# Kernel optimization log

Measured on AMD Instinct MI355X. Metric: run time of the kernel, lower is better.

## Reference

```python
import jax, jax.numpy as jnp
import numpy as np

N = 100000
F = 256
H = 128
C = 64
E = 1600000

def spmm(rows, cols, vals, h):
    # sparse [N,N] @ dense [N,D] via gather + segment-sum
    return jax.ops.segment_sum(vals[:, None] * h[cols], rows, num_segments=N)

def graph_conv(x, W, rows, cols, vals, b=None):
    # GraphConv: support = x @ W; out = adj @ support (+ bias)
    out = spmm(rows, cols, vals, x @ W)
    if b is not None:
        out = out + b
    return out

def setup_inputs() -> dict:
    key = jax.random.key(0)
    ks = jax.random.split(key, 20)
    d = {}
    d['x'] = jax.random.normal(ks[0], (N, F), dtype=jnp.float32)
    for i, name in enumerate(['mid', 'low', 'high']):
        d[name + '_rows'] = jax.random.randint(ks[1 + 3 * i], (E,), 0, N, dtype=jnp.int64 if jax.config.jax_enable_x64 else jnp.int32)
        d[name + '_cols'] = jax.random.randint(ks[2 + 3 * i], (E,), 0, N, dtype=jnp.int64 if jax.config.jax_enable_x64 else jnp.int32)
        d[name + '_vals'] = jax.random.uniform(ks[3 + 3 * i], (E,), dtype=jnp.float32) * 0.1
    s = lambda k, a, b_: jax.random.normal(k, (a, b_), dtype=jnp.float32) * (1.0 / np.sqrt(a))
    d['W_hid'] = s(ks[10], F, H)          # hidden_layers[0], no bias
    d['W_out'] = s(ks[11], H, C)          # out_layer
    d['b_out'] = jnp.zeros((C,), jnp.float32)
    d['W_low'] = s(ks[12], F, H)          # addHid_layer, no bias
    d['W_low_out'] = s(ks[13], H, C)      # addOut_layer
    d['b_low_out'] = jnp.zeros((C,), jnp.float32)
    d['W_high'] = s(ks[14], F, H)         # addHid_layer_HIGH, no bias
    d['W_high_out'] = s(ks[15], H, C)     # addOut_layer_HIGH
    d['b_high_out'] = jnp.zeros((C,), jnp.float32)
    d['gate2'] = jnp.array([0.5], jnp.float32)
    return d

def reference(x, mid_rows, mid_cols, mid_vals, low_rows, low_cols, low_vals,
              high_rows, high_cols, high_vals, W_hid, W_out, b_out,
              W_low, W_low_out, b_low_out, W_high, W_high_out, b_high_out, gate2):
    # dropout is identity at inference
    h = jax.nn.relu(graph_conv(x, W_hid, mid_rows, mid_cols, mid_vals))
    h = graph_conv(h, W_out, mid_rows, mid_cols, mid_vals, b_out)
    x2 = jax.nn.relu(graph_conv(x, W_low, low_rows, low_cols, low_vals))
    xh = jax.nn.relu(graph_conv(x, W_high, high_rows, high_cols, high_vals))
    x2 = graph_conv(x2, W_low_out, low_rows, low_cols, low_vals, b_low_out)
    xh = graph_conv(xh, W_high_out, high_rows, high_cols, high_vals, b_high_out)
    x_final = gate2 * h + (1.0 - gate2) * (x2 + xh)
    return jax.nn.log_softmax(x_final, axis=-1)
```

## Files before the change

### kernel.cpp

```cpp
#include <hip/hip_runtime.h>
#include <math.h>

#define NNODES 100000
#define NEDGES 1600000
#define FEAT 256
#define HID 128
#define NCLS 64
#define RPB 512
#define NBG 196
#define NB3 (3 * NBG)
#define CAP 8832
#define SC_CHUNK 8192
#define SC_THREADS 1024

typedef __attribute__((ext_vector_type(8))) short bf16x8;
typedef __attribute__((ext_vector_type(4))) float f32x4;
typedef __attribute__((ext_vector_type(2))) float f32x2;

__device__ __forceinline__ float bf2f(unsigned int u16) {
  union { unsigned int i; float f; } c; c.i = u16 << 16; return c.f;
}
__device__ __forceinline__ unsigned short f2bf(float f) {
  union { float f; unsigned int i; } c; c.f = f;
  unsigned int u = c.i;
  return (unsigned short)((u + 0x7fffu + ((u >> 16) & 1u)) >> 16);
}

__device__ __forceinline__ void fma8(const uint4 u, const f32x2 vv, f32x2* a) {
  f32x2 p0, p1, p2, p3;
  p0.x = __uint_as_float(u.x << 16); p0.y = __uint_as_float(u.x & 0xffff0000u);
  p1.x = __uint_as_float(u.y << 16); p1.y = __uint_as_float(u.y & 0xffff0000u);
  p2.x = __uint_as_float(u.z << 16); p2.y = __uint_as_float(u.z & 0xffff0000u);
  p3.x = __uint_as_float(u.w << 16); p3.y = __uint_as_float(u.w & 0xffff0000u);
  a[0] += p0 * vv; a[1] += p1 * vv; a[2] += p2 * vv; a[3] += p3 * vv;
}

__global__ __launch_bounds__(SC_THREADS) void k_bucket_scatter(
    const int* __restrict__ r0, const int* __restrict__ r1, const int* __restrict__ r2,
    const int* __restrict__ c0, const int* __restrict__ c1, const int* __restrict__ c2,
    const float* __restrict__ v0, const float* __restrict__ v1, const float* __restrict__ v2,
    int* __restrict__ gcur, int2* __restrict__ edges) {
  __shared__ int2 stage[SC_CHUNK];
  __shared__ unsigned char bid[SC_CHUNK];
  __shared__ int hist[NBG];
  __shared__ int lbase[NBG];
  __shared__ int gstart[NBG];
  __shared__ int cur[NBG];
  __shared__ int sd[2][256];
  int g = blockIdx.y;
  const int*   rr = (g == 0) ? r0 : (g == 1 ? r1 : r2);
  const int*   cc = (g == 0) ? c0 : (g == 1 ? c1 : c2);
  const float* vv = (g == 0) ? v0 : (g == 1 ? v1 : v2);
  int tid = threadIdx.x;
  int base = blockIdx.x * SC_CHUNK;
  int cnt_blk = NEDGES - base;
  if (cnt_blk > SC_CHUNK) cnt_blk = SC_CHUNK;

  for (int i = tid; i < NBG; i += SC_THREADS) hist[i] = 0;
  __syncthreads();

  int rowv[SC_CHUNK / SC_THREADS];
  int colv[SC_CHUNK / SC_THREADS];
  float valv[SC_CHUNK / SC_THREADS];
#pragma unroll
  for (int k = 0; k < SC_CHUNK / SC_THREADS; k++) {
    int e = base + k * SC_THREADS + tid;
    bool ok = e < NEDGES;
    rowv[k] = ok ? rr[e] : -1;
    colv[k] = ok ? cc[e] : 0;
    valv[k] = ok ? vv[e] : 0.f;
    if (ok) atomicAdd(&hist[rowv[k] >> 9], 1);
  }
  __syncthreads();

  if (tid < 256) sd[0][tid] = (tid < NBG) ? hist[tid] : 0;
  __syncthreads();
  int c = 0;
  for (int off = 1; off < 256; off <<= 1) {
    if (tid < 256) {
      int nv = sd[c][tid];
      if (tid >= off) nv += sd[c][tid - off];
      sd[c ^ 1][tid] = nv;
    }
    __syncthreads();
    c ^= 1;
  }
  if (tid < NBG) {
    int cn = hist[tid];
    int excl = sd[c][tid] - cn;
    lbase[tid] = excl;
    cur[tid] = excl;
    gstart[tid] = cn ? atomicAdd(&gcur[g * NBG + tid], cn) : 0;
  }
  __syncthreads();

#pragma unroll
  for (int k = 0; k < SC_CHUNK / SC_THREADS; k++) {
    if (rowv[k] >= 0) {
      int b = rowv[k] >> 9;
      int p = atomicAdd(&cur[b], 1);
      stage[p] = make_int2(((rowv[k] & (RPB - 1)) << 17) | colv[k], __float_as_int(valv[k]));
      bid[p] = (unsigned char)b;
    }
  }
  __syncthreads();

  for (int i = tid; i < cnt_blk; i += SC_THREADS) {
    int b = bid[i];
    int pos = gstart[b] + (i - lbase[b]);
    if (pos < CAP)
      edges[(size_t)(g * NBG + b) * CAP + pos] = stage[i];
  }
}

__global__ __launch_bounds__(512) void k_bucket_sort(const int* __restrict__ gcur,
                                                     int2* __restrict__ edges,
                                                     int* __restrict__ rps_all,
                                                     int* __restrict__ rpe_all) {
  __shared__ int2 stage[CAP];
  __shared__ int hist[RPB];
  __shared__ int sd[2][RPB];
  __shared__ int cur[RPB];
  int g = blockIdx.y, b = blockIdx.x;
  int tid = threadIdx.x;
  int idx = g * NBG + b;
  size_t base = (size_t)idx * CAP;
  int count = gcur[idx];
  if (count > CAP) count = CAP;
  hist[tid] = 0;
  __syncthreads();

  const int KSL = (CAP + 511) / 512;
  int2 ev[KSL];
#pragma unroll
  for (int k = 0; k < KSL; k++) {
    int i = tid + k * 512;
    if (i < count) {
      ev[k] = edges[base + i];
      atomicAdd(&hist[ev[k].x >> 17], 1);
    }
  }
  __syncthreads();

  int v = hist[tid];
  sd[0][tid] = v;
  __syncthreads();
  int c2 = 0;
  for (int off = 1; off < 512; off <<= 1) {
    int nv = sd[c2][tid];
    if (tid >= off) nv += sd[c2][tid - off];
    sd[c2 ^ 1][tid] = nv;
    __syncthreads();
    c2 ^= 1;
  }
  int excl = sd[c2][tid] - v;
  int row = b * RPB + tid;
  if (row < NNODES) {
    rps_all[g * NNODES + row] = (int)base + excl;
    rpe_all[g * NNODES + row] = (int)base + excl + v;
  }
  cur[tid] = excl;
  __syncthreads();

#pragma unroll
  for (int k = 0; k < KSL; k++) {
    int i = tid + k * 512;
    if (i < count) {
      int lr = ev[k].x >> 17;
      int p = atomicAdd(&cur[lr], 1);
      stage[p] = make_int2(ev[k].x & 0x1FFFF, ev[k].y);
    }
  }
  __syncthreads();

  for (int i = tid; i < count; i += 512) edges[base + i] = stage[i];
}

__global__ __launch_bounds__(256) void k_convert_bf16(const float* __restrict__ src,
                                                      unsigned short* __restrict__ dst,
                                                      int n4) {
  int i = blockIdx.x * blockDim.x + threadIdx.x;
  if (i < n4) {
    float4 v = ((const float4*)src)[i];
    ushort4 o;
    o.x = f2bf(v.x); o.y = f2bf(v.y); o.z = f2bf(v.z); o.w = f2bf(v.w);
    ((ushort4*)dst)[i] = o;
  }
}

__global__ __launch_bounds__(256) void k_transpose3(const float* __restrict__ s0,
                                                    const float* __restrict__ s1,
                                                    const float* __restrict__ s2,
                                                    unsigned short* __restrict__ d0,
                                                    unsigned short* __restrict__ d1,
                                                    unsigned short* __restrict__ d2,
                                                    int K, int N) {
  int g = blockIdx.y;
  const float* src = (g == 0) ? s0 : (g == 1 ? s1 : s2);
  unsigned short* dst = (g == 0) ? d0 : (g == 1 ? d1 : d2);
  int idx = blockIdx.x * 256 + threadIdx.x;
  if (idx < K * N) {
    int k = idx / N, n = idx % N;
    dst[(size_t)n * K + k] = f2bf(src[idx]);
  }
}

__global__ __launch_bounds__(256) void k_gemm1_b(const unsigned short* __restrict__ A,
                                                 const unsigned short* __restrict__ WtA,
                                                 unsigned short* __restrict__ C3, int M) {
  int bxy = blockIdx.x;
  int g = bxy % 3;
  int bx = bxy / 3;
  const unsigned short* Wt = WtA + (size_t)g * HID * FEAT;
  unsigned short* C = C3 + (size_t)g * M * HID;
  int tid = threadIdx.x;
  int wave = tid >> 6, lane = tid & 63;
  int quad = lane >> 4, r = lane & 15;
  int m0 = bx * 128 + wave * 32;
  int ra0 = m0 + r;      if (ra0 >= M) ra0 = 0;
  int ra1 = m0 + 16 + r; if (ra1 >= M) ra1 = 0;
  const unsigned short* pa0 = A + (size_t)ra0 * FEAT + quad * 8;
  const unsigned short* pa1 = A + (size_t)ra1 * FEAT + quad * 8;
  f32x4 acc[2][8];
#pragma unroll
  for (int i = 0; i < 2; i++)
#pragma unroll
    for (int j = 0; j < 8; j++) acc[i][j] = (f32x4){0.f, 0.f, 0.f, 0.f};
  for (int k0 = 0; k0 < FEAT; k0 += 32) {
    bf16x8 a0 = *(const bf16x8*)(pa0 + k0);
    bf16x8 a1 = *(const bf16x8*)(pa1 + k0);
#pragma unroll
    for (int nt = 0; nt < 8; nt++) {
      bf16x8 b = *(const bf16x8*)(Wt + (size_t)(nt * 16 + r) * FEAT + k0 + quad * 8);
      acc[0][nt] = __builtin_amdgcn_mfma_f32_16x16x32_bf16(a0, b, acc[0][nt], 0, 0, 0);
      acc[1][nt] = __builtin_amdgcn_mfma_f32_16x16x32_bf16(a1, b, acc[1][nt], 0, 0, 0);
    }
  }
#pragma unroll
  for (int t = 0; t < 2; t++)
#pragma unroll
    for (int reg = 0; reg < 4; reg++) {
      int row = m0 + t * 16 + quad * 4 + reg;
      if (row < M) {
#pragma unroll
        for (int nt = 0; nt < 8; nt++)
          C[(size_t)row * HID + nt * 16 + r] = f2bf(acc[t][nt][reg]);
      }
    }
}

__global__ __launch_bounds__(256) void k_gemm2_b(const unsigned short* __restrict__ A3,
                                                 const unsigned short* __restrict__ WtA,
                                                 unsigned short* __restrict__ C3, int M) {
  int g = blockIdx.y;
  const unsigned short* A = A3 + (size_t)g * M * HID;
  const unsigned short* Wt = WtA + (size_t)g * NCLS * HID;
  unsigned short* C = C3 + (size_t)g * M * NCLS;
  int tid = threadIdx.x;
  int wave = tid >> 6, lane = tid & 63;
  int quad = lane >> 4, r = lane & 15;
  int m0 = blockIdx.x * 128 + wave * 32;
  int ra0 = m0 + r;      if (ra0 >= M) ra0 = 0;
  int ra1 = m0 + 16 + r; if (ra1 >= M) ra1 = 0;
  const unsigned short* pa0 = A + (size_t)ra0 * HID + quad * 8;
  const unsigned short* pa1 = A + (size_t)ra1 * HID + quad * 8;
  f32x4 acc[2][4];
#pragma unroll
  for (int i = 0; i < 2; i++)
#pragma unroll
    for (int j = 0; j < 4; j++) acc[i][j] = (f32x4){0.f, 0.f, 0.f, 0.f};
  for (int k0 = 0; k0 < HID; k0 += 32) {
    bf16x8 a0 = *(const bf16x8*)(pa0 + k0);
    bf16x8 a1 = *(const bf16x8*)(pa1 + k0);
#pragma unroll
    for (int nt = 0; nt < 4; nt++) {
      bf16x8 b = *(const bf16x8*)(Wt + (size_t)(nt * 16 + r) * HID + k0 + quad * 8);
      acc[0][nt] = __builtin_amdgcn_mfma_f32_16x16x32_bf16(a0, b, acc[0][nt], 0, 0, 0);
      acc[1][nt] = __builtin_amdgcn_mfma_f32_16x16x32_bf16(a1, b, acc[1][nt], 0, 0, 0);
    }
  }
#pragma unroll
  for (int t = 0; t < 2; t++)
#pragma unroll
    for (int reg = 0; reg < 4; reg++) {
      int row = m0 + t * 16 + quad * 4 + reg;
      if (row < M) {
#pragma unroll
        for (int nt = 0; nt < 4; nt++)
          C[(size_t)row * NCLS + nt * 16 + r] = f2bf(acc[t][nt][reg]);
      }
    }
}

__global__ __launch_bounds__(256) void k_spmm128_b(const int* __restrict__ rps_all,
                                                   const int* __restrict__ rpe_all,
                                                   const int2* __restrict__ edges,
                                                   const unsigned short* __restrict__ dense3,
                                                   unsigned short* __restrict__ out3, int n) {
  int g = blockIdx.y;
  const int* rs = rps_all + (size_t)g * NNODES;
  const int* re = rpe_all + (size_t)g * NNODES;
  const unsigned short* dense = dense3 + (size_t)g * NNODES * HID;
  unsigned short* out = out3 + (size_t)g * NNODES * HID;
  int w = (blockIdx.x * blockDim.x + threadIdx.x) >> 6;
  int lane = threadIdx.x & 63;
  if (w >= n) return;
  int grp = lane >> 4;
  int sub = lane & 15;
  int s = rs[w], e = re[w];
  f32x2 a[4][4];
#pragma unroll
  for (int t = 0; t < 4; t++)
#pragma unroll
    for (int q = 0; q < 4; q++) a[t][q] = (f32x2){0.f, 0.f};
  for (int j = s; j < e; j += 16) {
    uint4 u[4];
    float f[4];
#pragma unroll
    for (int t = 0; t < 4; t++) {
      int ej = j + t * 4 + grp;
      bool ok = ej < e;
      int2 dd = edges[ok ? ej : s];
      u[t] = *(const uint4*)(dense + (size_t)dd.x * HID + sub * 8);
      f[t] = ok ? __int_as_float(dd.y) : 0.f;
    }
#pragma unroll
    for (int t = 0; t < 4; t++) {
      f32x2 vv; vv.x = f[t]; vv.y = f[t];
      fma8(u[t], vv, a[t]);
    }
  }
  unsigned int pk[4];
#pragma unroll
  for (int q = 0; q < 4; q++) {
    float lo = (a[0][q].x + a[1][q].x) + (a[2][q].x + a[3][q].x);
    float hi = (a[0][q].y + a[1][q].y) + (a[2][q].y + a[3][q].y);
    lo += __shfl_xor(lo, 32, 64); lo += __shfl_xor(lo, 16, 64);
    hi += __shfl_xor(hi, 32, 64); hi += __shfl_xor(hi, 16, 64);
    lo = fmaxf(lo, 0.f); hi = fmaxf(hi, 0.f);
    pk[q] = (unsigned int)f2bf(lo) | ((unsigned int)f2bf(hi) << 16);
  }
  if (lane < 16) {
    uint4 o; o.x = pk[0]; o.y = pk[1]; o.z = pk[2]; o.w = pk[3];
    *(uint4*)(out + (size_t)w * HID + sub * 8) = o;
  }
}

__global__ __launch_bounds__(256) void k_spmm64_final(const int* __restrict__ rps_all,
                                                      const int* __restrict__ rpe_all,
                                                      const int2* __restrict__ edges,
                                                      const unsigned short* __restrict__ dense3,
                                                      const float* __restrict__ b0p,
                                                      const float* __restrict__ b1p,
                                                      const float* __restrict__ b2p,
                                                      const float* __restrict__ gate,
                                                      float* __restrict__ outp, int n) {
  int w = (blockIdx.x * blockDim.x + threadIdx.x) >> 6;
  int lane = threadIdx.x & 63;
  if (w >= n) return;
  int grp = lane >> 3;
  int sub = lane & 7;
  float gv = gate[0];
  float omg = 1.0f - gv;
  float tot[8];
  {
    float4 x0 = *(const float4*)(b0p + sub * 8), x1 = *(const float4*)(b0p + sub * 8 + 4);
    float4 y0 = *(const float4*)(b1p + sub * 8), y1 = *(const float4*)(b1p + sub * 8 + 4);
    float4 z0 = *(const float4*)(b2p + sub * 8), z1 = *(const float4*)(b2p + sub * 8 + 4);
    tot[0] = gv * x0.x + omg * (y0.x + z0.x); tot[1] = gv * x0.y + omg * (y0.y + z0.y);
    tot[2] = gv * x0.z + omg * (y0.z + z0.z); tot[3] = gv * x0.w + omg * (y0.w + z0.w);
    tot[4] = gv * x1.x + omg * (y1.x + z1.x); tot[5] = gv * x1.y + omg * (y1.y + z1.y);
    tot[6] = gv * x1.z + omg * (y1.z + z1.z); tot[7] = gv * x1.w + omg * (y1.w + z1.w);
  }
  for (int g = 0; g < 3; g++) {
    const int* rs = rps_all + (size_t)g * NNODES;
    const int* re = rpe_all + (size_t)g * NNODES;
    const unsigned short* dense = dense3 + (size_t)g * NNODES * NCLS;
    int s = rs[w], e = re[w];
    f32x2 a0[4], a1[4];
#pragma unroll
    for (int q = 0; q < 4; q++) { a0[q] = (f32x2){0.f, 0.f}; a1[q] = (f32x2){0.f, 0.f}; }
    for (int j = s; j < e; j += 16) {
      int e0 = j + grp, e1 = j + 8 + grp;
      bool k0 = e0 < e, k1 = e1 < e;
      int2 d0 = edges[k0 ? e0 : s];
      int2 d1 = edges[k1 ? e1 : s];
      uint4 u0 = *(const uint4*)(dense + (size_t)d0.x * NCLS + sub * 8);
      uint4 u1 = *(const uint4*)(dense + (size_t)d1.x * NCLS + sub * 8);
      float f0 = k0 ? __int_as_float(d0.y) : 0.f;
      float f1 = k1 ? __int_as_float(d1.y) : 0.f;
      f32x2 v0; v0.x = f0; v0.y = f0;
      f32x2 v1; v1.x = f1; v1.y = f1;
      fma8(u0, v0, a0);
      fma8(u1, v1, a1);
    }
    float scale = (g == 0) ? gv : omg;
#pragma unroll
    for (int q = 0; q < 4; q++) {
      float lo = a0[q].x + a1[q].x;
      float hi = a0[q].y + a1[q].y;
      lo += __shfl_xor(lo, 32, 64); lo += __shfl_xor(lo, 16, 64); lo += __shfl_xor(lo, 8, 64);
      hi += __shfl_xor(hi, 32, 64); hi += __shfl_xor(hi, 16, 64); hi += __shfl_xor(hi, 8, 64);
      tot[2 * q] += scale * lo;
      tot[2 * q + 1] += scale * hi;
    }
  }
  float m = tot[0];
#pragma unroll
  for (int i = 1; i < 8; i++) m = fmaxf(m, tot[i]);
  m = fmaxf(m, __shfl_xor(m, 1, 64));
  m = fmaxf(m, __shfl_xor(m, 2, 64));
  m = fmaxf(m, __shfl_xor(m, 4, 64));
  float sum = 0.f;
#pragma unroll
  for (int i = 0; i < 8; i++) sum += expf(tot[i] - m);
  sum += __shfl_xor(sum, 1, 64);
  sum += __shfl_xor(sum, 2, 64);
  sum += __shfl_xor(sum, 4, 64);
  float ls = m + logf(sum);
  if (grp == 0) {
    size_t o = (size_t)w * NCLS + sub * 8;
    *(float4*)(outp + o)     = make_float4(tot[0] - ls, tot[1] - ls, tot[2] - ls, tot[3] - ls);
    *(float4*)(outp + o + 4) = make_float4(tot[4] - ls, tot[5] - ls, tot[6] - ls, tot[7] - ls);
  }
}

extern "C" void kernel_launch(void* const* d_in, const int* in_sizes, int n_in,
                              void* d_out, int out_size, void* d_ws, size_t ws_size,
                              hipStream_t stream) {
  (void)in_sizes; (void)n_in; (void)out_size; (void)ws_size;
  const float* x = (const float*)d_in[0];
  const int*   rows[3]   = {(const int*)d_in[1], (const int*)d_in[4], (const int*)d_in[7]};
  const int*   colsIn[3] = {(const int*)d_in[2], (const int*)d_in[5], (const int*)d_in[8]};
  const float* valsIn[3] = {(const float*)d_in[3], (const float*)d_in[6], (const float*)d_in[9]};
  const float* Whid[3] = {(const float*)d_in[10], (const float*)d_in[13], (const float*)d_in[16]};
  const float* Wout[3] = {(const float*)d_in[11], (const float*)d_in[14], (const float*)d_in[17]};
  const float* bout[3] = {(const float*)d_in[12], (const float*)d_in[15], (const float*)d_in[18]};
  const float* gate = (const float*)d_in[19];
  float* out = (float*)d_out;

  const int N = NNODES, E = NEDGES;
  size_t off = 0;
  auto ws = [&](size_t bytes) {
    void* p = (char*)d_ws + off;
    off += (bytes + 255) & ~(size_t)255;
    return p;
  };
  unsigned short* R1 = (unsigned short*)ws((size_t)3 * N * HID * 2);
  unsigned short* x_bf = R1;
  unsigned short* h13  = R1;
  unsigned short* hsup3 = (unsigned short*)ws((size_t)3 * N * HID * 2);
  unsigned short* Wt1a = (unsigned short*)ws((size_t)3 * HID * FEAT * 2);
  unsigned short* Wt2a = (unsigned short*)ws((size_t)3 * NCLS * HID * 2);
  int2* edges   = (int2*)ws((size_t)NB3 * CAP * 8);
  int*  rps_all = (int*) ws((size_t)3 * N * 4);
  int*  rpe_all = (int*) ws((size_t)3 * N * 4);
  int*  gcur    = (int*) ws(NB3 * 4);

  dim3 b256(256);
  dim3 gRows3((N + 3) / 4, 3);
  int nbGemm = (N + 127) / 128;

  k_convert_bf16<<<(N * FEAT / 4 + 255) / 256, b256, 0, stream>>>(x, x_bf, N * FEAT / 4);
  k_transpose3<<<dim3((FEAT * HID + 255) / 256, 3), b256, 0, stream>>>(
      Whid[0], Whid[1], Whid[2], Wt1a, Wt1a + (size_t)HID * FEAT, Wt1a + (size_t)2 * HID * FEAT,
      FEAT, HID);
  k_transpose3<<<dim3((HID * NCLS + 255) / 256, 3), b256, 0, stream>>>(
      Wout[0], Wout[1], Wout[2], Wt2a, Wt2a + (size_t)NCLS * HID, Wt2a + (size_t)2 * NCLS * HID,
      HID, NCLS);

  hipMemsetAsync(gcur, 0, NB3 * 4, stream);
  k_bucket_scatter<<<dim3((E + SC_CHUNK - 1) / SC_CHUNK, 3), dim3(SC_THREADS), 0, stream>>>(
      rows[0], rows[1], rows[2], colsIn[0], colsIn[1], colsIn[2],
      valsIn[0], valsIn[1], valsIn[2], gcur, edges);
  k_bucket_sort<<<dim3(NBG, 3), 512, 0, stream>>>(gcur, edges, rps_all, rpe_all);

  k_gemm1_b<<<dim3(3 * nbGemm), b256, 0, stream>>>(x_bf, Wt1a, hsup3, N);
  k_spmm128_b<<<gRows3, b256, 0, stream>>>(rps_all, rpe_all, edges, hsup3, h13, N);
  k_gemm2_b<<<dim3(nbGemm, 3), b256, 0, stream>>>(h13, Wt2a, hsup3, N);
  k_spmm64_final<<<gRows3.x == 0 ? dim3(1) : dim3((N + 3) / 4), b256, 0, stream>>>(
      rps_all, rpe_all, edges, hsup3, bout[0], bout[1], bout[2], gate, out, N);
}
```

Measured before the change: 753.0 us.

## Pad CSR row segments to multiples of eight to remove SpMM tail predication

```diff
diff --git a/kernel.cpp b/kernel.cpp
--- a/kernel.cpp
+++ b/kernel.cpp
@@ -10,6 +10,7 @@
 #define NBG 196
 #define NB3 (3 * NBG)
 #define CAP 8832
+#define CAPP 12416
 #define SC_CHUNK 8192
 #define SC_THREADS 1024
 
@@ -108,8 +109,8 @@
   for (int i = tid; i < cnt_blk; i += SC_THREADS) {
     int b = bid[i];
     int pos = gstart[b] + (i - lbase[b]);
-    if (pos < CAP)
-      edges[(size_t)(g * NBG + b) * CAP + pos] = stage[i];
+    if (pos < CAPP)
+      edges[(size_t)(g * NBG + b) * CAPP + pos] = stage[i];
   }
 }
 
@@ -117,20 +118,21 @@
                                                      int2* __restrict__ edges,
                                                      int* __restrict__ rps_all,
                                                      int* __restrict__ rpe_all) {
-  __shared__ int2 stage[CAP];
+  __shared__ int2 stage[CAPP];
   __shared__ int hist[RPB];
   __shared__ int sd[2][RPB];
   __shared__ int cur[RPB];
+  __shared__ int ptot_s;
   int g = blockIdx.y, b = blockIdx.x;
   int tid = threadIdx.x;
   int idx = g * NBG + b;
-  size_t base = (size_t)idx * CAP;
+  size_t base = (size_t)idx * CAPP;
   int count = gcur[idx];
-  if (count > CAP) count = CAP;
+  if (count > CAPP) count = CAPP;
   hist[tid] = 0;
   __syncthreads();
 
-  const int KSL = (CAP + 511) / 512;
+  const int KSL = (CAPP + 511) / 512;
   int2 ev[KSL];
 #pragma unroll
   for (int k = 0; k < KSL; k++) {
@@ -143,7 +145,8 @@
   __syncthreads();
 
   int v = hist[tid];
-  sd[0][tid] = v;
+  int pv = (v + 7) & ~7;
+  sd[0][tid] = pv;
   __syncthreads();
   int c2 = 0;
   for (int off = 1; off < 512; off <<= 1) {
@@ -153,13 +156,14 @@
     __syncthreads();
     c2 ^= 1;
   }
-  int excl = sd[c2][tid] - v;
+  int pexcl = sd[c2][tid] - pv;
+  if (tid == 511) ptot_s = sd[c2][511];
   int row = b * RPB + tid;
   if (row < NNODES) {
-    rps_all[g * NNODES + row] = (int)base + excl;
-    rpe_all[g * NNODES + row] = (int)base + excl + v;
-  }
-  cur[tid] = excl;
+    rps_all[g * NNODES + row] = (int)base + pexcl;
+    rpe_all[g * NNODES + row] = (int)base + pexcl + pv;
+  }
+  cur[tid] = pexcl;
   __syncthreads();
 
 #pragma unroll
@@ -168,12 +172,16 @@
     if (i < count) {
       int lr = ev[k].x >> 17;
       int p = atomicAdd(&cur[lr], 1);
-      stage[p] = make_int2(ev[k].x & 0x1FFFF, ev[k].y);
-    }
-  }
-  __syncthreads();
-
-  for (int i = tid; i < count; i += 512) edges[base + i] = stage[i];
+      if (p < CAPP) stage[p] = make_int2(ev[k].x & 0x1FFFF, ev[k].y);
+    }
+  }
+  for (int i = pexcl + v; i < pexcl + pv; i++)
+    if (i < CAPP) stage[i] = make_int2(0, 0);
+  __syncthreads();
+
+  int ptot = ptot_s;
+  if (ptot > CAPP) ptot = CAPP;
+  for (int i = tid; i < ptot; i += 512) edges[base + i] = stage[i];
 }
 
 __global__ __launch_bounds__(256) void k_convert_bf16(const float* __restrict__ src,
@@ -307,34 +315,26 @@
   if (w >= n) return;
   int grp = lane >> 4;
   int sub = lane & 15;
-  int s = rs[w], e = re[w];
-  f32x2 a[4][4];
-#pragma unroll
-  for (int t = 0; t < 4; t++)
-#pragma unroll
-    for (int q = 0; q < 4; q++) a[t][q] = (f32x2){0.f, 0.f};
-  for (int j = s; j < e; j += 16) {
-    uint4 u[4];
-    float f[4];
-#pragma unroll
-    for (int t = 0; t < 4; t++) {
-      int ej = j + t * 4 + grp;
-      bool ok = ej < e;
-      int2 dd = edges[ok ? ej : s];
-      u[t] = *(const uint4*)(dense + (size_t)dd.x * HID + sub * 8);
-      f[t] = ok ? __int_as_float(dd.y) : 0.f;
-    }
-#pragma unroll
-    for (int t = 0; t < 4; t++) {
-      f32x2 vv; vv.x = f[t]; vv.y = f[t];
-      fma8(u[t], vv, a[t]);
-    }
+  int s = __builtin_amdgcn_readfirstlane(rs[w]);
+  int e = __builtin_amdgcn_readfirstlane(re[w]);
+  f32x2 a0[4], a1[4];
+#pragma unroll
+  for (int q = 0; q < 4; q++) { a0[q] = (f32x2){0.f, 0.f}; a1[q] = (f32x2){0.f, 0.f}; }
+  for (int j = s; j < e; j += 8) {
+    int2 d0 = edges[j + grp];
+    int2 d1 = edges[j + 4 + grp];
+    uint4 u0 = *(const uint4*)(dense + (size_t)d0.x * HID + sub * 8);
+    uint4 u1 = *(const uint4*)(dense + (size_t)d1.x * HID + sub * 8);
+    f32x2 v0; v0.x = __int_as_float(d0.y); v0.y = v0.x;
+    f32x2 v1; v1.x = __int_as_float(d1.y); v1.y = v1.x;
+    fma8(u0, v0, a0);
+    fma8(u1, v1, a1);
   }
   unsigned int pk[4];
 #pragma unroll
   for (int q = 0; q < 4; q++) {
-    float lo = (a[0][q].x + a[1][q].x) + (a[2][q].x + a[3][q].x);
-    float hi = (a[0][q].y + a[1][q].y) + (a[2][q].y + a[3][q].y);
+    float lo = a0[q].x + a1[q].x;
+    float hi = a0[q].y + a1[q].y;
     lo += __shfl_xor(lo, 32, 64); lo += __shfl_xor(lo, 16, 64);
     hi += __shfl_xor(hi, 32, 64); hi += __shfl_xor(hi, 16, 64);
     lo = fmaxf(lo, 0.f); hi = fmaxf(hi, 0.f);
@@ -376,23 +376,27 @@
     const int* rs = rps_all + (size_t)g * NNODES;
     const int* re = rpe_all + (size_t)g * NNODES;
     const unsigned short* dense = dense3 + (size_t)g * NNODES * NCLS;
-    int s = rs[w], e = re[w];
+    int s = __builtin_amdgcn_readfirstlane(rs[w]);
+    int e = __builtin_amdgcn_readfirstlane(re[w]);
     f32x2 a0[4], a1[4];
 #pragma unroll
     for (int q = 0; q < 4; q++) { a0[q] = (f32x2){0.f, 0.f}; a1[q] = (f32x2){0.f, 0.f}; }
-    for (int j = s; j < e; j += 16) {
-      int e0 = j + grp, e1 = j + 8 + grp;
-      bool k0 = e0 < e, k1 = e1 < e;
-      int2 d0 = edges[k0 ? e0 : s];
-      int2 d1 = edges[k1 ? e1 : s];
+    int j = s;
+    for (; j + 16 <= e; j += 16) {
+      int2 d0 = edges[j + grp];
+      int2 d1 = edges[j + 8 + grp];
       uint4 u0 = *(const uint4*)(dense + (size_t)d0.x * NCLS + sub * 8);
       uint4 u1 = *(const uint4*)(dense + (size_t)d1.x * NCLS + sub * 8);
-      float f0 = k0 ? __int_as_float(d0.y) : 0.f;
-      float f1 = k1 ? __int_as_float(d1.y) : 0.f;
-      f32x2 v0; v0.x = f0; v0.y = f0;
-      f32x2 v1; v1.x = f1; v1.y = f1;
+      f32x2 v0; v0.x = __int_as_float(d0.y); v0.y = v0.x;
+      f32x2 v1; v1.x = __int_as_float(d1.y); v1.y = v1.x;
       fma8(u0, v0, a0);
       fma8(u1, v1, a1);
+    }
+    if (j < e) {
+      int2 d0 = edges[j + grp];
+      uint4 u0 = *(const uint4*)(dense + (size_t)d0.x * NCLS + sub * 8);
+      f32x2 v0; v0.x = __int_as_float(d0.y); v0.y = v0.x;
+      fma8(u0, v0, a0);
     }
     float scale = (g == 0) ? gv : omg;
 #pragma unroll
@@ -452,7 +456,7 @@
   unsigned short* hsup3 = (unsigned short*)ws((size_t)3 * N * HID * 2);
   unsigned short* Wt1a = (unsigned short*)ws((size_t)3 * HID * FEAT * 2);
   unsigned short* Wt2a = (unsigned short*)ws((size_t)3 * NCLS * HID * 2);
-  int2* edges   = (int2*)ws((size_t)NB3 * CAP * 8);
+  int2* edges   = (int2*)ws((size_t)NB3 * CAPP * 8);
   int*  rps_all = (int*) ws((size_t)3 * N * 4);
   int*  rpe_all = (int*) ws((size_t)3 * N * 4);
   int*  gcur    = (int*) ws(NB3 * 4);
@@ -478,6 +482,6 @@
   k_gemm1_b<<<dim3(3 * nbGemm), b256, 0, stream>>>(x_bf, Wt1a, hsup3, N);
   k_spmm128_b<<<gRows3, b256, 0, stream>>>(rps_all, rpe_all, edges, hsup3, h13, N);
   k_gemm2_b<<<dim3(nbGemm, 3), b256, 0, stream>>>(h13, Wt2a, hsup3, N);
-  k_spmm64_final<<<gRows3.x == 0 ? dim3(1) : dim3((N + 3) / 4), b256, 0, stream>>>(
+  k_spmm64_final<<<dim3((N + 3) / 4), b256, 0, stream>>>(
       rps_all, rpe_all, edges, hsup3, bout[0], bout[1], bout[2], gate, out, N);
 }
```

Measured after the change: 746.9 us. About the same (-0.8%).
